# Kernel tuning notes

Hardware: AMD Instinct MI355X
Metric: run time of the kernel (lower is better)

## Reference

```python
import jax, jax.numpy as jnp
import numpy as np

NEG_BIG = -9e15
ALPHA = 0.2  # leakyrelu negative slope

N, F_IN, F_OUT = 8192, 512, 64


def setup_inputs() -> dict:
    key = jax.random.key(0)
    k1, k2, k3, k4 = jax.random.split(key, 4)
    input = jax.random.normal(k1, (N, F_IN), dtype=jnp.float32)
    adj = jax.random.randint(k2, (N, N), 0, 2, dtype=jnp.int32)
    W = jax.random.normal(k3, (F_IN, F_OUT), dtype=jnp.float32) * 0.05
    a = jax.random.normal(k4, (2 * F_OUT, 1), dtype=jnp.float32) * 0.1
    return {"input": input, "adj": adj, "W": W, "a": a}


def reference(input, adj, W, a):
    # h: [N, F_out]
    h = input @ W
    # The original builds a_input[i,j] = concat(h_i, h_j) and dots with a.
    # Decompose: e_ij = leakyrelu(h_i @ a_src + h_j @ a_dst) -- identical math,
    # avoids the N*N*2F intermediate.
    a_src = a[:F_OUT, 0]  # [F_out]
    a_dst = a[F_OUT:, 0]  # [F_out]
    s_src = h @ a_src     # [N]
    s_dst = h @ a_dst     # [N]
    e = jax.nn.leaky_relu(s_src[:, None] + s_dst[None, :], negative_slope=ALPHA)  # [N, N]
    masked = jnp.where(adj > 0, e, jnp.float32(NEG_BIG))
    attention = jax.nn.softmax(masked, axis=1)  # dropout omitted (eval mode)
    h_prime = attention @ h  # [N, F_out]
    return jax.nn.elu(h_prime)  # concat=True
```

## Files before the change

### kernel.cpp

```cpp
#include <hip/hip_runtime.h>
#include <hip/hip_bf16.h>

namespace {
constexpr int kN    = 8192;
constexpr int kFin  = 512;
constexpr int kFout = 64;
constexpr float kAlpha = 0.2f;
constexpr int kJSplit = 8;
constexpr int kJLen   = kN / kJSplit;
constexpr int kChunks = kJLen / 32;
constexpr int kTileParts = 2;

using bf16x4 = __attribute__((ext_vector_type(4))) short;
using bf16x8 = __attribute__((ext_vector_type(8))) short;
using f32x4  = __attribute__((ext_vector_type(4))) float;

__device__ __forceinline__ unsigned short f2bf(float x) {
  return __builtin_bit_cast(unsigned short, __float2bfloat16(x));
}
__device__ __forceinline__ float lrelu(float x) {
  return fmaxf(x, kAlpha * x);
}
__device__ __forceinline__ unsigned int fkey(float x) {
  unsigned int b = __float_as_uint(x);
  return (b & 0x80000000u) ? ~b : (b | 0x80000000u);
}
__device__ __forceinline__ float fdec(unsigned int k) {
  return (k & 0x80000000u) ? __uint_as_float(k ^ 0x80000000u) : __uint_as_float(~k);
}
}

__global__ __launch_bounds__(256) void k_wt(const float* __restrict__ W,
                                            float* __restrict__ WT2,
                                            unsigned int* __restrict__ Smax_u) {
  const int gid = blockIdx.x * 256 + threadIdx.x;
  if (gid == 0) *Smax_u = 0u;
  const int k = gid >> 6, f = gid & 63;
  WT2[(k >> 2) * 256 + f * 4 + (k & 3)] = W[gid];
}

__global__ __launch_bounds__(256) void k_linear(
    const float* __restrict__ X, const float* __restrict__ WT2, const float* __restrict__ A,
    unsigned short* __restrict__ hTf, float* __restrict__ s_src, float* __restrict__ s_dst,
    unsigned int* __restrict__ Smax_u)
{
  const int t = threadIdx.x;
  const int wv = t >> 6, f = t & 63;
  const int i0 = blockIdx.x * 16;

  __shared__ float Xlds[16 * kFin];
  __shared__ unsigned short h_sm[16][64];
  __shared__ float red[4];

  {
    const float4* Xg = (const float4*)(X + (size_t)i0 * kFin);
    float4* Xl = (float4*)Xlds;
    float4 v0 = Xg[t +   0], v1 = Xg[t + 256], v2 = Xg[t +  512], v3 = Xg[t +  768];
    float4 v4 = Xg[t +1024], v5 = Xg[t +1280], v6 = Xg[t + 1536], v7 = Xg[t + 1792];
    Xl[t +    0] = v0; Xl[t +  256] = v1; Xl[t +  512] = v2; Xl[t +  768] = v3;
    Xl[t + 1024] = v4; Xl[t + 1280] = v5; Xl[t + 1536] = v6; Xl[t + 1792] = v7;
  }
  __syncthreads();

  const int r0l = wv * 4;
  const float4* wp = (const float4*)WT2 + f;
  float acc0 = 0.f, acc1 = 0.f, acc2 = 0.f, acc3 = 0.f;
  float4 wb0 = wp[0];
  float4 wb1 = wp[64];
  const float* xr = Xlds + r0l * kFin;
  for (int k = 0; k < kFin; k += 4) {
    const float4 wc = (k & 4) ? wb1 : wb0;
    if (k + 8 < kFin) {
      const float4 wn = wp[(size_t)(k + 8) * 16];
      if (k & 4) wb1 = wn; else wb0 = wn;
    }
    const float4 xa = *(const float4*)(xr + k);
    const float4 xb = *(const float4*)(xr + kFin + k);
    const float4 xc = *(const float4*)(xr + 2 * kFin + k);
    const float4 xd = *(const float4*)(xr + 3 * kFin + k);
#pragma unroll
    for (int j = 0; j < 4; ++j) {
      const float wk = ((const float*)&wc)[j];
      acc0 = fmaf(((const float*)&xa)[j], wk, acc0);
      acc1 = fmaf(((const float*)&xb)[j], wk, acc1);
      acc2 = fmaf(((const float*)&xc)[j], wk, acc2);
      acc3 = fmaf(((const float*)&xd)[j], wk, acc3);
    }
  }

  const float asrc = A[f], adst = A[kFout + f];
  float accs[4] = {acc0, acc1, acc2, acc3};
  float dmax = -3.4e38f;
#pragma unroll
  for (int r = 0; r < 4; ++r) {
    float vs = accs[r] * asrc;
    float vd = accs[r] * adst;
#pragma unroll
    for (int off = 32; off > 0; off >>= 1) {
      vs += __shfl_xor(vs, off, 64);
      vd += __shfl_xor(vd, off, 64);
    }
    if (f == 0) {
      s_src[i0 + r0l + r] = vs;
      s_dst[i0 + r0l + r] = vd;
      dmax = fmaxf(dmax, vd);
    }
    h_sm[r0l + r][f] = f2bf(accs[r]);
  }
  if (f == 0) red[wv] = dmax;
  __syncthreads();
  if (t == 0) {
    float m = fmaxf(fmaxf(red[0], red[1]), fmaxf(red[2], red[3]));
    atomicMax(Smax_u, fkey(m));
  }

  if (t < 128) {
    const int jblk = i0 >> 5, half = (i0 >> 4) & 1;
    const int w = t >> 5, li = t & 31;
    const int lane = half * 32 + li;
    const int ql = li >> 4, fcol = w * 16 + (li & 15);
    bf16x8 v;
#pragma unroll
    for (int e = 0; e < 8; ++e) v[e] = (short)h_sm[ql * 8 + e][fcol];
    *(bf16x8*)(hTf + (size_t)jblk * 2048 + w * 512 + (size_t)lane * 8) = v;
  }
}

__global__ __launch_bounds__(256, 4) void k_attn(
    const int* __restrict__ adj, const unsigned short* __restrict__ hTf,
    const float* __restrict__ s_src, const float* __restrict__ s_dst,
    const unsigned int* __restrict__ Smax_u, float* __restrict__ accp,
    float* __restrict__ lp)
{
  const int t = threadIdx.x;
  const int wv = t >> 6, lane = t & 63;
  const int wid = blockIdx.x * 4 + wv;
  const int tile = wid >> 3;
  const int q    = wid & 7;
  const int i0 = tile * 16, jbase = q * kJLen;
  const int lr = lane >> 3;
  const int lg = lane & 7;
  const int row = lane & 15, quad = lane >> 4;

  __shared__ unsigned short Pl[4][2][16][40];
  __shared__ float sacc[4][16][64];
  __shared__ float sl[4][16];

  const float S = fdec(*Smax_u);
  const float sA = s_src[i0 + lr];
  const float sB = s_src[i0 + 8 + lr];
  const float mA = lrelu(sA + S);
  const float mB = lrelu(sB + S);

  const int4* aA = (const int4*)(adj + (size_t)(i0 + lr) * kN + jbase) + lg;
  const int4* aB = (const int4*)(adj + (size_t)(i0 + 8 + lr) * kN + jbase) + lg;
  const float4* dp = (const float4*)(s_dst + jbase) + lg;
  const unsigned short* hbase = hTf + (size_t)(jbase >> 5) * 2048 + (size_t)lane * 8;

  float l_accA = 0.f, l_accB = 0.f;
  f32x4 acc0 = {0.f, 0.f, 0.f, 0.f};
  f32x4 acc1 = {0.f, 0.f, 0.f, 0.f};
  f32x4 acc2 = {0.f, 0.f, 0.f, 0.f};
  f32x4 acc3 = {0.f, 0.f, 0.f, 0.f};

  int4   Aa = aA[0], Ba = aB[0];  float4 Da = dp[0];
  int4   Ab = aA[8], Bb = aB[8];  float4 Db = dp[8];

  auto body = [&](int c, int sbuf, int4& A, int4& B, float4& D)
      __attribute__((always_inline)) {
    const unsigned short* hp = hbase + (size_t)c * 2048;
    const uint4 hv0 = *(const uint4*)(hp +    0);
    const uint4 hv1 = *(const uint4*)(hp +  512);
    const uint4 hv2 = *(const uint4*)(hp + 1024);
    const uint4 hv3 = *(const uint4*)(hp + 1536);

    float pvA[4], pvB[4];
    {
      const int*   ia = (const int*)&A;
      const int*   ib = (const int*)&B;
      const float* dd = (const float*)&D;
#pragma unroll
      for (int j = 0; j < 4; ++j) {
        const float eA = lrelu(sA + dd[j]);
        const float eB = lrelu(sB + dd[j]);
        pvA[j] = ia[j] > 0 ? __expf(eA - mA) : 0.f;
        pvB[j] = ib[j] > 0 ? __expf(eB - mB) : 0.f;
      }
    }
    l_accA += (pvA[0] + pvA[1]) + (pvA[2] + pvA[3]);
    l_accB += (pvB[0] + pvB[1]) + (pvB[2] + pvB[3]);

    bf16x4 wA, wB;
#pragma unroll
    for (int j = 0; j < 4; ++j) {
      wA[j] = (short)f2bf(pvA[j]);
      wB[j] = (short)f2bf(pvB[j]);
    }
    *(bf16x4*)&Pl[wv][sbuf][lr][lg * 4]     = wA;
    *(bf16x4*)&Pl[wv][sbuf][8 + lr][lg * 4] = wB;

    {
      const int cn = (c + 2) & (kChunks - 1);
      A = aA[cn * 8];  B = aB[cn * 8];  D = dp[cn * 8];
    }

    const bf16x8 pa = *(const bf16x8*)&Pl[wv][sbuf][row][quad * 8];
    __builtin_amdgcn_s_setprio(1);
    acc0 = __builtin_amdgcn_mfma_f32_16x16x32_bf16(pa, __builtin_bit_cast(bf16x8, hv0), acc0, 0, 0, 0);
    acc1 = __builtin_amdgcn_mfma_f32_16x16x32_bf16(pa, __builtin_bit_cast(bf16x8, hv1), acc1, 0, 0, 0);
    acc2 = __builtin_amdgcn_mfma_f32_16x16x32_bf16(pa, __builtin_bit_cast(bf16x8, hv2), acc2, 0, 0, 0);
    acc3 = __builtin_amdgcn_mfma_f32_16x16x32_bf16(pa, __builtin_bit_cast(bf16x8, hv3), acc3, 0, 0, 0);
    __builtin_amdgcn_s_setprio(0);
  };

  for (int c = 0; c < kChunks; c += 2) {
    body(c,     0, Aa, Ba, Da);
    body(c + 1, 1, Ab, Bb, Db);
  }

  l_accA += __shfl_xor(l_accA, 1, 64);
  l_accA += __shfl_xor(l_accA, 2, 64);
  l_accA += __shfl_xor(l_accA, 4, 64);
  l_accB += __shfl_xor(l_accB, 1, 64);
  l_accB += __shfl_xor(l_accB, 2, 64);
  l_accB += __shfl_xor(l_accB, 4, 64);
  if (lg == 0) {
    sl[wv][lr]     = l_accA;
    sl[wv][8 + lr] = l_accB;
  }

  {
    float* ab = &sacc[wv][0][0];
#pragma unroll
    for (int reg = 0; reg < 4; ++reg) {
      ab[(quad * 4 + reg) * 64 +  0 + row] = acc0[reg];
      ab[(quad * 4 + reg) * 64 + 16 + row] = acc1[reg];
      ab[(quad * 4 + reg) * 64 + 32 + row] = acc2[reg];
      ab[(quad * 4 + reg) * 64 + 48 + row] = acc3[reg];
    }
  }
  __syncthreads();

  {
    const float* sb = &sacc[0][0][0];
    float* gout = accp + (size_t)blockIdx.x * 16 * 64;
#pragma unroll
    for (int k = 0; k < 4; ++k) {
      const int idx = t + k * 256;
      gout[idx] = (sb[idx] + sb[1024 + idx]) + (sb[2048 + idx] + sb[3072 + idx]);
    }
    if (t < 16) {
      lp[(size_t)blockIdx.x * 16 + t] =
          (sl[0][t] + sl[1][t]) + (sl[2][t] + sl[3][t]);
    }
  }
}

__global__ __launch_bounds__(256) void k_comb(const float* __restrict__ accp,
                                              const float* __restrict__ lp,
                                              float* __restrict__ out)
{
  const int gid = blockIdx.x * 256 + threadIdx.x;
  const int i = gid >> 6, f = gid & 63;
  const int ib = i >> 4, il = i & 15;
  const int b0 = ib * kTileParts;
  float a = 0.f, l = 0.f;
#pragma unroll
  for (int p = 0; p < kTileParts; ++p) {
    a += accp[((size_t)(b0 + p) * 16 + il) * 64 + f];
    l += lp[(size_t)(b0 + p) * 16 + il];
  }
  float v = a / l;
  v = v > 0.f ? v : __expf(v) - 1.f;
  out[gid] = v;
}

extern "C" void kernel_launch(void* const* d_in, const int* in_sizes, int n_in,
                              void* d_out, int out_size, void* d_ws, size_t ws_size,
                              hipStream_t stream) {
  const float* X   = (const float*)d_in[0];
  const int*   adj = (const int*)d_in[1];
  const float* W   = (const float*)d_in[2];
  const float* A   = (const float*)d_in[3];
  float* out = (float*)d_out;

  char* ws = (char*)d_ws;
  unsigned short* hTf = (unsigned short*)ws;  ws += (size_t)kN * kFout * 2;
  float* WT2   = (float*)ws;                  ws += (size_t)kFout * kFin * 4;
  float* s_src = (float*)ws;                  ws += kN * 4;
  float* s_dst = (float*)ws;                  ws += kN * 4;
  unsigned int* Smax_u = (unsigned int*)ws;   ws += 256;
  float* accp  = (float*)ws;                  ws += (size_t)(kN / 16) * kTileParts * 16 * 64 * 4;
  float* lp    = (float*)ws;

  k_wt    <<<kFin * kFout / 256, 256, 0, stream>>>(W, WT2, Smax_u);
  k_linear<<<kN / 16, 256, 0, stream>>>(X, WT2, A, hTf, s_src, s_dst, Smax_u);
  k_attn  <<<(kN / 16) * kJSplit / 4, 256, 0, stream>>>(adj, hTf, s_src, s_dst, Smax_u, accp, lp);
  k_comb  <<<kN * kFout / 256, 256, 0, stream>>>(accp, lp, out);
}
```

Before: 431.0 us.

## Split attention j-range finer and alias per-wave LDS buffers to raise occupancy

Doubles the number of column segments per row tile, so each wave handles a shorter j-range and the grid has twice as many blocks. The combine kernel now reduces four partials per tile instead of two. The separate P, accumulator and row-sum shared arrays are overlaid into one 4160-byte slot per wave, cutting LDS per block so the launch bound can request 8 blocks per CU. This trades more partial-sum traffic and a longer combine for more parallelism and better latency hiding on the adj stream.

```diff
diff --git a/kernel.cpp b/kernel.cpp
--- a/kernel.cpp
+++ b/kernel.cpp
@@ -6,10 +6,10 @@
 constexpr int kFin  = 512;
 constexpr int kFout = 64;
 constexpr float kAlpha = 0.2f;
-constexpr int kJSplit = 8;
+constexpr int kJSplit = 16;
 constexpr int kJLen   = kN / kJSplit;
 constexpr int kChunks = kJLen / 32;
-constexpr int kTileParts = 2;
+constexpr int kTileParts = 4;
 
 using bf16x4 = __attribute__((ext_vector_type(4))) short;
 using bf16x8 = __attribute__((ext_vector_type(8))) short;
@@ -64,10 +64,10 @@
 
   const int r0l = wv * 4;
   const float4* wp = (const float4*)WT2 + f;
+  const float* xr = Xlds + r0l * kFin;
   float acc0 = 0.f, acc1 = 0.f, acc2 = 0.f, acc3 = 0.f;
   float4 wb0 = wp[0];
   float4 wb1 = wp[64];
-  const float* xr = Xlds + r0l * kFin;
   for (int k = 0; k < kFin; k += 4) {
     const float4 wc = (k & 4) ? wb1 : wb0;
     if (k + 8 < kFin) {
@@ -126,7 +126,7 @@
   }
 }
 
-__global__ __launch_bounds__(256, 4) void k_attn(
+__global__ __launch_bounds__(256, 8) void k_attn(
     const int* __restrict__ adj, const unsigned short* __restrict__ hTf,
     const float* __restrict__ s_src, const float* __restrict__ s_dst,
     const unsigned int* __restrict__ Smax_u, float* __restrict__ accp,
@@ -135,16 +135,16 @@
   const int t = threadIdx.x;
   const int wv = t >> 6, lane = t & 63;
   const int wid = blockIdx.x * 4 + wv;
-  const int tile = wid >> 3;
-  const int q    = wid & 7;
-  const int i0 = tile * 16, jbase = q * kJLen;
+  const int tile = wid >> 4;
+  const int seg  = wid & 15;
+  const int i0 = tile * 16, jbase = seg * kJLen;
   const int lr = lane >> 3;
   const int lg = lane & 7;
   const int row = lane & 15, quad = lane >> 4;
 
-  __shared__ unsigned short Pl[4][2][16][40];
-  __shared__ float sacc[4][16][64];
-  __shared__ float sl[4][16];
+  __shared__ __align__(16) char smem[4 * 4160];
+  char* slot = smem + wv * 4160;
+  unsigned short (*Plw)[16][40] = (unsigned short (*)[16][40])slot;
 
   const float S = fdec(*Smax_u);
   const float sA = s_src[i0 + lr];
@@ -196,15 +196,15 @@
       wA[j] = (short)f2bf(pvA[j]);
       wB[j] = (short)f2bf(pvB[j]);
     }
-    *(bf16x4*)&Pl[wv][sbuf][lr][lg * 4]     = wA;
-    *(bf16x4*)&Pl[wv][sbuf][8 + lr][lg * 4] = wB;
+    *(bf16x4*)&Plw[sbuf][lr][lg * 4]     = wA;
+    *(bf16x4*)&Plw[sbuf][8 + lr][lg * 4] = wB;
 
     {
       const int cn = (c + 2) & (kChunks - 1);
       A = aA[cn * 8];  B = aB[cn * 8];  D = dp[cn * 8];
     }
 
-    const bf16x8 pa = *(const bf16x8*)&Pl[wv][sbuf][row][quad * 8];
+    const bf16x8 pa = *(const bf16x8*)&Plw[sbuf][row][quad * 8];
     __builtin_amdgcn_s_setprio(1);
     acc0 = __builtin_amdgcn_mfma_f32_16x16x32_bf16(pa, __builtin_bit_cast(bf16x8, hv0), acc0, 0, 0, 0);
     acc1 = __builtin_amdgcn_mfma_f32_16x16x32_bf16(pa, __builtin_bit_cast(bf16x8, hv1), acc1, 0, 0, 0);
@@ -225,12 +225,13 @@
   l_accB += __shfl_xor(l_accB, 2, 64);
   l_accB += __shfl_xor(l_accB, 4, 64);
   if (lg == 0) {
-    sl[wv][lr]     = l_accA;
-    sl[wv][8 + lr] = l_accB;
+    float* slw = (float*)(slot + 4096);
+    slw[lr]     = l_accA;
+    slw[8 + lr] = l_accB;
   }
 
   {
-    float* ab = &sacc[wv][0][0];
+    float* ab = (float*)slot;
 #pragma unroll
     for (int reg = 0; reg < 4; ++reg) {
       ab[(quad * 4 + reg) * 64 +  0 + row] = acc0[reg];
@@ -242,16 +243,20 @@
   __syncthreads();
 
   {
-    const float* sb = &sacc[0][0][0];
     float* gout = accp + (size_t)blockIdx.x * 16 * 64;
 #pragma unroll
     for (int k = 0; k < 4; ++k) {
       const int idx = t + k * 256;
-      gout[idx] = (sb[idx] + sb[1024 + idx]) + (sb[2048 + idx] + sb[3072 + idx]);
+      float s = 0.f;
+#pragma unroll
+      for (int w = 0; w < 4; ++w) s += ((const float*)(smem + w * 4160))[idx];
+      gout[idx] = s;
     }
     if (t < 16) {
-      lp[(size_t)blockIdx.x * 16 + t] =
-          (sl[0][t] + sl[1][t]) + (sl[2][t] + sl[3][t]);
+      float s = 0.f;
+#pragma unroll
+      for (int w = 0; w < 4; ++w) s += ((const float*)(smem + w * 4160 + 4096))[t];
+      lp[(size_t)blockIdx.x * 16 + t] = s;
     }
   }
 }
@@ -295,6 +300,6 @@
 
   k_wt    <<<kFin * kFout / 256, 256, 0, stream>>>(W, WT2, Smax_u);
   k_linear<<<kN / 16, 256, 0, stream>>>(X, WT2, A, hTf, s_src, s_dst, Smax_u);
-  k_attn  <<<(kN / 16) * kJSplit / 4, 256, 0, stream>>>(adj, hTf, s_src, s_dst, Smax_u, accp, lp);
+  k_attn  <<<(kN / 16) * kTileParts, 256, 0, stream>>>(adj, hTf, s_src, s_dst, Smax_u, accp, lp);
   k_comb  <<<kN * kFout / 256, 256, 0, stream>>>(accp, lp, out);
 }
```

After: 627.8 us. +45.7%, slower.
